# Kernel optimization log

Hardware: AMD Instinct MI355X
Metric: run time of the kernel (lower is better)

## Reference

```python
import jax, jax.numpy as jnp
import numpy as np

B, T, D, H, E, S, K = 2, 2048, 768, 1536, 8, 1, 2
STD = 0.02


def setup_inputs() -> dict:
    key = jax.random.key(0)
    ks = jax.random.split(key, 8)
    x = jax.random.normal(ks[0], (B, T, D), jnp.float32)
    router_w = jax.random.normal(ks[1], (E, D), jnp.float32) * STD
    sw1 = jax.random.normal(ks[2], (S, D, H), jnp.float32) * STD
    sw2 = jax.random.normal(ks[3], (S, D, H), jnp.float32) * STD
    sproj = jax.random.normal(ks[4], (S, H, D), jnp.float32) * STD
    ew1 = jax.random.normal(ks[5], (E, D, H), jnp.float32) * STD
    ew2 = jax.random.normal(ks[6], (E, D, H), jnp.float32) * STD
    eproj = jax.random.normal(ks[7], (E, H, D), jnp.float32) * STD
    return {"x": x, "router_w": router_w, "sw1": sw1, "sw2": sw2,
            "sproj": sproj, "ew1": ew1, "ew2": ew2, "eproj": eproj,
            "top_k": K}


def reference(x, router_w, sw1, sw2, sproj, ew1, ew2, eproj, top_k):
    n_experts = router_w.shape[0]
    # Shared experts (SwiGLU), summed over the shared-expert axis s.
    a = jnp.einsum('btd,sdh->bsth', x, sw1)
    b = jnp.einsum('btd,sdh->bsth', x, sw2)
    shared_out = jnp.einsum('bsth,shd->btd', jax.nn.silu(a) * b, sproj)  # [B,T,D]

    # Router: note the original applies softmax and calls the result `logits`,
    # returning it as the second output.
    probs = jax.nn.softmax(jnp.einsum('btd,ed->bte', x, router_w), axis=-1)  # [B,T,E]
    top_vals, top_idx = jax.lax.top_k(probs, top_k)
    weights = top_vals / jnp.sum(top_vals, axis=-1, keepdims=True)  # renormalized [B,T,K]

    # Dense combine weights: combine[b,t,e] = sum_k weights[b,t,k] * 1[top_idx[b,t,k]==e]
    combine = jnp.sum(jax.nn.one_hot(top_idx, n_experts, dtype=x.dtype)
                      * weights[..., None], axis=-2)  # [B,T,E]

    # Routed experts: compute every expert densely, then mask/weight by combine.
    ea = jnp.einsum('btd,edh->bteh', x, ew1)
    eb = jnp.einsum('btd,edh->bteh', x, ew2)
    routed = jnp.einsum('bteh,ehd,bte->btd', jax.nn.silu(ea) * eb, eproj, combine)

    return shared_out + routed, probs
```

## Files before the change

kernel.cpp:

```cpp
#include <hip/hip_runtime.h>

typedef unsigned short u16;
typedef __bf16 bf16x8 __attribute__((ext_vector_type(8)));
typedef float f32x4 __attribute__((ext_vector_type(4)));

__device__ __forceinline__ u16 f2bf(float f) {
  union { float f; unsigned u; } v; v.f = f;
  return (u16)((v.u + 0x7fffu + ((v.u >> 16) & 1u)) >> 16);
}

#define GLDS16(g, l)                                                          \
  __builtin_amdgcn_global_load_lds(                                           \
      (const __attribute__((address_space(1))) void*)(g),                     \
      (__attribute__((address_space(3))) void*)(l), 16, 0, 0)

#define SBAR()  __builtin_amdgcn_s_barrier()
#define SCHED() __builtin_amdgcn_sched_barrier(0)
#define VMCNT(n) asm volatile("s_waitcnt vmcnt(" #n ")" ::: "memory")

#define NTOK 4096
#define DIM  768
#define HID  1536
#define NEXP 8
#define CAPR 10240
#define SHB  10240
#define NSLOT 14336
#define MAXT1 56
#define MAXT2 112

__global__ __launch_bounds__(256) void k_tr_all(const float* __restrict__ ew1,
                                                const float* __restrict__ sw1,
                                                const float* __restrict__ ew2,
                                                const float* __restrict__ sw2,
                                                const float* __restrict__ eproj,
                                                const float* __restrict__ sproj,
                                                u16* __restrict__ dstBase) {
  __shared__ u16 tile[64][65];
  constexpr size_t SL = (size_t)HID * DIM;
  const int z = blockIdx.z;
  const float* src;
  int R, C, bxx = blockIdx.x, byy = blockIdx.y;
  if (z < 9)       { src = (z < 8) ? ew1 + (size_t)z * SL : sw1; R = DIM; C = HID; }
  else if (z < 18) { const int q = z - 9;  src = (q < 8) ? ew2 + (size_t)q * SL : sw2; R = DIM; C = HID; }
  else             { const int q = z - 18; src = (q < 8) ? eproj + (size_t)q * SL : sproj;
                     R = HID; C = DIM; const int t = bxx; bxx = byy; byy = t; }
  u16* dst = dstBase + (size_t)z * SL;
  const int c0 = bxx * 64, r0 = byy * 64;
  const int tx = threadIdx.x, ty = threadIdx.y;
  #pragma unroll
  for (int i = 0; i < 16; i++)
    tile[ty + 4 * i][tx] = f2bf(src[(size_t)(r0 + ty + 4 * i) * C + c0 + tx]);
  __syncthreads();
  #pragma unroll
  for (int i = 0; i < 16; i++)
    dst[(size_t)(c0 + ty + 4 * i) * R + r0 + tx] = tile[tx][ty + 4 * i];
}

__global__ __launch_bounds__(64) void k_router(const float* __restrict__ x,
                                               const float* __restrict__ rw,
                                               float* __restrict__ probs,
                                               int* __restrict__ topIdx,
                                               float* __restrict__ topW,
                                               u16* __restrict__ xb) {
  const int t = blockIdx.x;
  const int lane = threadIdx.x;
  const float* xr = x + (size_t)t * DIM;
  u16* xbr = xb + (size_t)t * DIM;
  float acc[NEXP] = {0, 0, 0, 0, 0, 0, 0, 0};
  #pragma unroll
  for (int i = 0; i < DIM / 64; i++) {
    const int d = lane + 64 * i;
    const float xv = xr[d];
    xbr[d] = f2bf(xv);
    #pragma unroll
    for (int e = 0; e < NEXP; e++) acc[e] += xv * rw[e * DIM + d];
  }
  #pragma unroll
  for (int e = 0; e < NEXP; e++)
    #pragma unroll
    for (int s = 32; s > 0; s >>= 1) acc[e] += __shfl_xor(acc[e], s, 64);
  if (lane == 0) {
    float mx = acc[0];
    #pragma unroll
    for (int e = 1; e < NEXP; e++) mx = fmaxf(mx, acc[e]);
    float p[NEXP], sum = 0.f;
    #pragma unroll
    for (int e = 0; e < NEXP; e++) { p[e] = expf(acc[e] - mx); sum += p[e]; }
    const float inv = 1.f / sum;
    #pragma unroll
    for (int e = 0; e < NEXP; e++) p[e] *= inv;
    #pragma unroll
    for (int e = 0; e < NEXP; e++) probs[(size_t)t * NEXP + e] = p[e];
    int i1 = 0;
    #pragma unroll
    for (int e = 1; e < NEXP; e++) if (p[e] > p[i1]) i1 = e;
    int i2 = (i1 == 0) ? 1 : 0;
    #pragma unroll
    for (int e = 0; e < NEXP; e++) if (e != i1 && p[e] > p[i2]) i2 = e;
    const float s2 = 1.f / (p[i1] + p[i2]);
    topIdx[2 * t] = i1; topIdx[2 * t + 1] = i2;
    topW[2 * t] = p[i1] * s2; topW[2 * t + 1] = p[i2] * s2;
  }
}

__global__ __launch_bounds__(256) void k_build(const int* __restrict__ topIdx,
                                               const float* __restrict__ topW,
                                               int* __restrict__ listT,
                                               float* __restrict__ listW,
                                               int* __restrict__ listP,
                                               int* __restrict__ cnt) {
  const int e = blockIdx.x;
  const int tid = threadIdx.x, w = tid >> 6, lane = tid & 63;
  __shared__ int wt[4];
  int base = 0;
  for (int c = 0; c < NTOK / 256; ++c) {
    const int t = c * 256 + tid;
    const int i0 = topIdx[2 * t], i1 = topIdx[2 * t + 1];
    const int pr = (i0 == e) ? 1 : ((i1 == e) ? 2 : 0);
    const unsigned long long m = __ballot(pr != 0);
    const int wl = __popcll(m & ((1ull << lane) - 1ull));
    if (lane == 0) wt[w] = __popcll(m);
    __syncthreads();
    int wbase = 0;
    #pragma unroll
    for (int j = 0; j < 4; j++) if (j < w) wbase += wt[j];
    if (pr) {
      const int pos = base + wbase + wl;
      listT[e * NTOK + pos] = t;
      listW[e * NTOK + pos] = (pr == 1) ? topW[2 * t] : topW[2 * t + 1];
      listP[e * NTOK + pos] = pr;
    }
    base += wt[0] + wt[1] + wt[2] + wt[3];
    __syncthreads();
  }
  if (tid == 0) cnt[e] = base;
}

__global__ __launch_bounds__(256) void k_tilemap(const int* __restrict__ cnt,
                                                 const int* __restrict__ listT,
                                                 const float* __restrict__ listW,
                                                 const int* __restrict__ listP,
                                                 int* __restrict__ tE1, int* __restrict__ tM1,
                                                 int* __restrict__ tE2, int* __restrict__ tM2,
                                                 int* __restrict__ slotTok,
                                                 float* __restrict__ slotW,
                                                 int* __restrict__ tokSlot) {
  __shared__ int offPad[NEXP + 1];
  __shared__ int cs[NEXP];
  const int tid = threadIdx.x;
  if (tid == 0) {
    int tt = 0, acc = 0;
    for (int e = 0; e < NEXP; e++) {
      cs[e] = cnt[e];
      offPad[e] = acc;
      const int tiles = (cs[e] + 255) >> 8;
      for (int i = 0; i < tiles; i++) { tE1[tt] = e; tM1[tt] = acc + i * 256; tt++; }
      acc += tiles * 256;
    }
    offPad[NEXP] = acc;
    for (int i = 0; i < NTOK / 256; i++) { tE1[tt] = NEXP; tM1[tt] = SHB + i * 256; tt++; }
    for (; tt < MAXT1; tt++) { tE1[tt] = -1; tM1[tt] = 0; }
    for (int j = 0; j < MAXT1; j++) {
      tE2[2 * j] = tE1[j];     tM2[2 * j] = tM1[j];
      tE2[2 * j + 1] = tE1[j]; tM2[2 * j + 1] = tM1[j] + 128;
    }
  }
  __syncthreads();
  for (int s = tid; s < CAPR; s += 256) {
    int tok = 0; float wv = 0.f; int pp = 0;
    #pragma unroll
    for (int e = 0; e < NEXP; e++)
      if (s >= offPad[e] && s < offPad[e + 1]) {
        const int i = s - offPad[e];
        if (i < cs[e]) {
          tok = listT[e * NTOK + i];
          wv = listW[e * NTOK + i];
          pp = listP[e * NTOK + i];
        }
      }
    slotTok[s] = tok; slotW[s] = wv;
    if (pp) tokSlot[2 * tok + (pp - 1)] = s;
  }
  for (int s = tid; s < NTOK; s += 256) { slotTok[SHB + s] = s; slotW[SHB + s] = 1.f; }
}

__global__ __launch_bounds__(512, 2) void k_gemm1(const u16* __restrict__ xb,
                                                  const u16* __restrict__ w1t,
                                                  const u16* __restrict__ w2t,
                                                  const int* __restrict__ tE1,
                                                  const int* __restrict__ tM1,
                                                  const int* __restrict__ slotTok,
                                                  const float* __restrict__ slotW,
                                                  u16* __restrict__ hidden) {
  __shared__ alignas(16) u16 L[2][32768];
  const int bid = blockIdx.x;
  const int wgid = (bid & 7) * 84 + (bid >> 3);
  const int bx = wgid % MAXT1, by = wgid / MAXT1;
  const int e = tE1[bx];
  if (e < 0) return;
  const int m0 = tM1[bx];
  const int nBase = by * 128;
  constexpr size_t SL = (size_t)HID * DIM;
  const u16* w1 = w1t + (size_t)e * SL;
  const u16* w2 = w2t + (size_t)e * SL;
  const int tid = threadIdx.x, w = tid >> 6, lane = tid & 63;
  const int wr = w >> 1, wc = w & 1;

  const int srow = tid >> 2;
  const int kcol = ((tid & 3) ^ ((tid >> 3) & 3)) * 8;
  const int tokA0 = slotTok[m0 + srow];
  const int tokA1 = slotTok[m0 + 128 + srow];
  const u16* gA0 = xb + (size_t)tokA0 * DIM + kcol;
  const u16* gA1 = xb + (size_t)tokA1 * DIM + kcol;
  const u16* gB1 = w1 + (size_t)(nBase + srow) * DIM + kcol;
  const u16* gB2 = w2 + (size_t)(nBase + srow) * DIM + kcol;
  const int dA0 = tid * 8, dA1 = 4096 + tid * 8, dB = tid * 8;

  const int rl = lane & 15;
  const int kq = lane >> 4;
  const int aBase = (wr * 64 + rl) * 32 + (kq ^ ((rl >> 1) & 3)) * 8;
  const int bBase = (wc * 64 + rl) * 32 + (kq ^ ((rl >> 1) & 3)) * 8;

  f32x4 acc1[4][4], acc2[4][4];
  const f32x4 vz = {0.f, 0.f, 0.f, 0.f};
  #pragma unroll
  for (int m = 0; m < 4; m++)
    #pragma unroll
    for (int n = 0; n < 4; n++) { acc1[m][n] = vz; acc2[m][n] = vz; }

#define G1_STA(d, koff, kh) do {                                              \
    GLDS16(gA0 + (koff), &L[d][(kh) * 8192 + dA0]);                           \
    GLDS16(gA1 + (koff), &L[d][(kh) * 8192 + dA1]); } while (0)
#define G1_STB(d, koff, kh) do {                                              \
    GLDS16(gB1 + (koff), &L[d][16384 + (kh) * 4096 + dB]);                    \
    GLDS16(gB2 + (koff), &L[d][24576 + (kh) * 4096 + dB]); } while (0)
#define G1_RDB(d, kh) do { _Pragma("unroll")                                  \
    for (int n = 0; n < 4; n++) {                                             \
      b1v[n] = *(const bf16x8*)&L[d][16384 + (kh) * 4096 + bBase + n * 512];  \
      b2v[n] = *(const bf16x8*)&L[d][24576 + (kh) * 4096 + bBase + n * 512]; } } while (0)
#define G1_RDA(d, kh, mp) do { _Pragma("unroll")                              \
    for (int j = 0; j < 2; j++)                                               \
      av[j] = *(const bf16x8*)&L[d][(kh) * 8192 + aBase + ((mp) * 2 + j) * 512]; } while (0)
#define G1_MM(mp) do { __builtin_amdgcn_s_setprio(1);                         \
    _Pragma("unroll") for (int j = 0; j < 2; j++)                             \
      _Pragma("unroll") for (int n = 0; n < 4; n++) {                         \
        acc1[(mp) * 2 + j][n] = __builtin_amdgcn_mfma_f32_16x16x32_bf16(av[j], b1v[n], acc1[(mp) * 2 + j][n], 0, 0, 0); \
        acc2[(mp) * 2 + j][n] = __builtin_amdgcn_mfma_f32_16x16x32_bf16(av[j], b2v[n], acc2[(mp) * 2 + j][n], 0, 0, 0); } \
    __builtin_amdgcn_s_setprio(0); } while (0)

  G1_STA(0, 0, 0);  G1_STB(0, 0, 0);
  G1_STA(0, 32, 1); G1_STB(0, 32, 1);
  G1_STA(1, 64, 0); G1_STB(1, 64, 0);
  SCHED(); VMCNT(8); SBAR(); SCHED();

  bf16x8 av[2], b1v[4], b2v[4];
  for (int i = 0; i < 5; i++) {
    const int kOff = i * 128;
    G1_RDB(0, 0); G1_RDA(0, 0, 0); SCHED(); G1_STA(1, kOff + 96, 1); SCHED();
    G1_MM(0); SCHED(); SBAR(); SCHED();
    G1_RDA(0, 0, 1); SCHED(); G1_STB(1, kOff + 96, 1); SCHED();
    G1_MM(1); SCHED(); VMCNT(8); SBAR(); SCHED();
    G1_RDB(0, 1); G1_RDA(0, 1, 0); SCHED(); G1_STA(0, kOff + 128, 0); SCHED();
    G1_MM(0); SCHED(); SBAR(); SCHED();
    G1_RDA(0, 1, 1); SCHED(); G1_STB(0, kOff + 128, 0); SCHED();
    G1_MM(1); SCHED(); VMCNT(8); SBAR(); SCHED();
    G1_RDB(1, 0); G1_RDA(1, 0, 0); SCHED(); G1_STA(0, kOff + 160, 1); SCHED();
    G1_MM(0); SCHED(); SBAR(); SCHED();
    G1_RDA(1, 0, 1); SCHED(); G1_STB(0, kOff + 160, 1); SCHED();
    G1_MM(1); SCHED(); VMCNT(8); SBAR(); SCHED();
    G1_RDB(1, 1); G1_RDA(1, 1, 0); SCHED(); G1_STA(1, kOff + 192, 0); SCHED();
    G1_MM(0); SCHED(); SBAR(); SCHED();
    G1_RDA(1, 1, 1); SCHED(); G1_STB(1, kOff + 192, 0); SCHED();
    G1_MM(1); SCHED(); VMCNT(8); SBAR(); SCHED();
  }
  G1_RDB(0, 0); G1_RDA(0, 0, 0); SCHED(); G1_STA(1, 736, 1); SCHED();
  G1_MM(0); SCHED(); SBAR(); SCHED();
  G1_RDA(0, 0, 1); SCHED(); G1_STB(1, 736, 1); SCHED();
  G1_MM(1); SCHED(); VMCNT(8); SBAR(); SCHED();
  G1_RDB(0, 1); G1_RDA(0, 1, 0); SCHED(); G1_MM(0); SCHED(); SBAR(); SCHED();
  G1_RDA(0, 1, 1); SCHED(); G1_MM(1); SCHED(); VMCNT(4); SBAR(); SCHED();
  G1_RDB(1, 0); G1_RDA(1, 0, 0); SCHED(); G1_MM(0); SCHED(); SBAR(); SCHED();
  G1_RDA(1, 0, 1); SCHED(); G1_MM(1); SCHED(); VMCNT(0); SBAR(); SCHED();
  G1_RDB(1, 1); G1_RDA(1, 1, 0); SCHED(); G1_MM(0); SCHED(); SBAR(); SCHED();
  G1_RDA(1, 1, 1); SCHED(); G1_MM(1);
#undef G1_STA
#undef G1_STB
#undef G1_RDB
#undef G1_RDA
#undef G1_MM

  #pragma unroll
  for (int m = 0; m < 4; m++)
    #pragma unroll
    for (int r = 0; r < 4; r++) {
      const int slot = m0 + wr * 64 + m * 16 + (lane >> 4) * 4 + r;
      const float cwv = slotW[slot];
      #pragma unroll
      for (int n = 0; n < 4; n++) {
        const int hcol = nBase + wc * 64 + n * 16 + (lane & 15);
        const float v1 = acc1[m][n][r], v2 = acc2[m][n][r];
        hidden[(size_t)slot * HID + hcol] = f2bf((v1 / (1.f + __expf(-v1))) * v2 * cwv);
      }
    }
}

__global__ __launch_bounds__(256, 3) void k_gemm2(const u16* __restrict__ hid,
                                                  const u16* __restrict__ pjt,
                                                  const int* __restrict__ tE2,
                                                  const int* __restrict__ tM2,
                                                  float* __restrict__ g2) {
  __shared__ alignas(16) u16 As[3][4096];
  __shared__ alignas(16) u16 Bs[3][4096];
  const int bid = blockIdx.x;
  const int wgid = (bid & 7) * 84 + (bid >> 3);
  const int bx = wgid % MAXT2;
  const int by = wgid / MAXT2;
  const int e = tE2[bx];
  if (e < 0) return;
  const int m0 = tM2[bx];
  const int nBase = by * 128;
  constexpr size_t SL = (size_t)HID * DIM;
  const u16* pj = pjt + (size_t)e * SL;
  const int tid = threadIdx.x, w = tid >> 6, lane = tid & 63;
  const int wr = w >> 1, wc = w & 1;

  const int qrow = lane >> 2;
  const int col0 = ((lane & 3) ^ ((lane >> 3) & 3)) * 8;
  const u16* gA0 = hid + (size_t)(m0 + w * 32 + qrow) * HID + col0;
  const u16* gA1 = hid + (size_t)(m0 + w * 32 + 16 + qrow) * HID + col0;
  const u16* gBa = pj + (size_t)(nBase + w * 32 + qrow) * HID + col0;
  const u16* gBb = pj + (size_t)(nBase + w * 32 + 16 + qrow) * HID + col0;
  const int l0 = (w * 128 + lane) * 8, l1 = (w * 128 + lane + 64) * 8;

  f32x4 acc[4][4];
  const f32x4 vz = {0.f, 0.f, 0.f, 0.f};
  #pragma unroll
  for (int m = 0; m < 4; m++)
    #pragma unroll
    for (int n = 0; n < 4; n++) acc[m][n] = vz;

  const int rbase = lane & 15;
  const int swz = (lane >> 4) ^ ((rbase >> 1) & 3);
  const int aoffB = (wr * 64 + rbase) * 32 + swz * 8;
  const int boffB = (wc * 64 + rbase) * 32 + swz * 8;

#define G2_STAGE(buf, kk) do {                                                \
    GLDS16(gA0 + (kk), &As[buf][l0]); GLDS16(gA1 + (kk), &As[buf][l1]);       \
    GLDS16(gBa + (kk), &Bs[buf][l0]); GLDS16(gBb + (kk), &Bs[buf][l1]);       \
  } while (0)

#define G2_BODY(buf, vm, dostage, kk) do {                                    \
    SCHED(); VMCNT(vm); SBAR(); SCHED();                                      \
    if (dostage) { G2_STAGE((buf + 2) % 3, kk); SCHED(); }                    \
    bf16x8 av[4], bv[4];                                                      \
    _Pragma("unroll")                                                         \
    for (int m = 0; m < 4; m++) av[m] = *(const bf16x8*)&As[buf][aoffB + m * 512]; \
    _Pragma("unroll")                                                         \
    for (int n = 0; n < 4; n++) bv[n] = *(const bf16x8*)&Bs[buf][boffB + n * 512]; \
    __builtin_amdgcn_s_setprio(1);                                            \
    _Pragma("unroll")                                                         \
    for (int m = 0; m < 4; m++)                                               \
      _Pragma("unroll")                                                       \
      for (int n = 0; n < 4; n++)                                             \
        acc[m][n] = __builtin_amdgcn_mfma_f32_16x16x32_bf16(av[m], bv[n], acc[m][n], 0, 0, 0); \
    __builtin_amdgcn_s_setprio(0);                                            \
  } while (0)

  G2_STAGE(0, 0);  SCHED();
  G2_STAGE(1, 32); SCHED();
  for (int t = 0; t < 45; t += 3) {
    G2_BODY(0, 4, true, (t + 2) * 32);
    G2_BODY(1, 4, true, (t + 3) * 32);
    G2_BODY(2, 4, true, (t + 4) * 32);
  }
  G2_BODY(0, 4, true, 47 * 32);
  G2_BODY(1, 4, false, 0);
  G2_BODY(2, 0, false, 0);
#undef G2_BODY
#undef G2_STAGE

  #pragma unroll
  for (int m = 0; m < 4; m++)
    #pragma unroll
    for (int r = 0; r < 4; r++) {
      const int slot = m0 + wr * 64 + m * 16 + (lane >> 4) * 4 + r;
      #pragma unroll
      for (int n = 0; n < 4; n++) {
        const int dcol = nBase + wc * 64 + n * 16 + (lane & 15);
        g2[(size_t)slot * DIM + dcol] = acc[m][n][r];
      }
    }
}

__global__ __launch_bounds__(192) void k_combine(const float* __restrict__ g2,
                                                 const int* __restrict__ tokSlot,
                                                 float* __restrict__ out) {
  const int t = blockIdx.x, d4 = threadIdx.x;
  const int sA = tokSlot[2 * t], sB = tokSlot[2 * t + 1];
  const int lo = sA < sB ? sA : sB;
  const int hi = sA < sB ? sB : sA;
  const float4 a = ((const float4*)(g2 + (size_t)lo * DIM))[d4];
  const float4 b = ((const float4*)(g2 + (size_t)hi * DIM))[d4];
  const float4 c = ((const float4*)(g2 + (size_t)(SHB + t) * DIM))[d4];
  float4 o;
  o.x = a.x + b.x + c.x; o.y = a.y + b.y + c.y;
  o.z = a.z + b.z + c.z; o.w = a.w + b.w + c.w;
  ((float4*)(out + (size_t)t * DIM))[d4] = o;
}

extern "C" void kernel_launch(void* const* d_in, const int* in_sizes, int n_in,
                              void* d_out, int out_size, void* d_ws, size_t ws_size,
                              hipStream_t stream) {
  const float* x     = (const float*)d_in[0];
  const float* rw    = (const float*)d_in[1];
  const float* sw1   = (const float*)d_in[2];
  const float* sw2   = (const float*)d_in[3];
  const float* sproj = (const float*)d_in[4];
  const float* ew1   = (const float*)d_in[5];
  const float* ew2   = (const float*)d_in[6];
  const float* eproj = (const float*)d_in[7];
  float* out   = (float*)d_out;
  float* probs = out + (size_t)NTOK * DIM;

  constexpr size_t SL = (size_t)HID * DIM;
  constexpr size_t off_xb   = 0;
  constexpr size_t off_w1t  = 6291456;
  constexpr size_t off_w2t  = off_w1t + 2 * 9 * SL;
  constexpr size_t off_pjt  = off_w2t + 2 * 9 * SL;
  constexpr size_t off_hid  = off_pjt + 2 * 9 * SL;
  constexpr size_t off_g2   = off_hid + (size_t)NSLOT * HID * 2;
  constexpr size_t off_meta = off_g2 + (size_t)NSLOT * DIM * 4;

  char* ws = (char*)d_ws;
  u16*   xb   = (u16*)(ws + off_xb);
  u16*   w1t  = (u16*)(ws + off_w1t);
  u16*   w2t  = (u16*)(ws + off_w2t);
  u16*   pjt  = (u16*)(ws + off_pjt);
  u16*   hid  = (u16*)(ws + off_hid);
  float* g2   = (float*)(ws + off_g2);
  char*  meta = ws + off_meta;
  int*   topIdx  = (int*)meta;
  float* topW    = (float*)(meta + 32768);
  int*   listT   = (int*)(meta + 65536);
  float* listW   = (float*)(meta + 196608);
  int*   listP   = (int*)(meta + 327680);
  int*   cnt     = (int*)(meta + 458752);
  int*   tE1     = (int*)(meta + 459264);
  int*   tM1     = (int*)(meta + 459776);
  int*   tE2     = (int*)(meta + 460288);
  int*   tM2     = (int*)(meta + 460800);
  int*   slotTok = (int*)(meta + 461312);
  float* slotW   = (float*)(meta + 518656);
  int*   tokSlot = (int*)(meta + 576000);

  k_router<<<NTOK, 64, 0, stream>>>(x, rw, probs, topIdx, topW, xb);
  k_tr_all<<<dim3(HID / 64, DIM / 64, 27), dim3(64, 4), 0, stream>>>(
      ew1, sw1, ew2, sw2, eproj, sproj, w1t);

  k_build<<<NEXP, 256, 0, stream>>>(topIdx, topW, listT, listW, listP, cnt);
  k_tilemap<<<1, 256, 0, stream>>>(cnt, listT, listW, listP, tE1, tM1, tE2, tM2,
                                   slotTok, slotW, tokSlot);

  k_gemm1<<<MAXT1 * (HID / 128), 512, 0, stream>>>(xb, w1t, w2t, tE1, tM1,
                                                   slotTok, slotW, hid);
  k_gemm2<<<MAXT2 * (DIM / 128), 256, 0, stream>>>(hid, pjt, tE2, tM2, g2);
  k_combine<<<NTOK, 192, 0, stream>>>(g2, tokSlot, out);
}
```

Baseline: 215.3 us.

## Repipeline gemm2 with split-K double buffering, parallelize slot map, pack router

The gemm2 kernel drops the 3-stage 32-wide K pipeline and uses two 64-wide K buffers, each split into two halves. Loads for later halves are interleaved with MFMA work at a finer grain, and occupancy drops from 3 to 2 blocks per CU. The single-block tilemap kernel is split into a tiny map kernel plus a multi-block slot-fill kernel, so slot filling no longer runs on one workgroup. The router now packs four tokens per 256-thread block, which cuts the block count.

```diff
diff --git a/kernel.cpp b/kernel.cpp
--- a/kernel.cpp
+++ b/kernel.cpp
@@ -56,14 +56,14 @@
     dst[(size_t)(c0 + ty + 4 * i) * R + r0 + tx] = tile[tx][ty + 4 * i];
 }
 
-__global__ __launch_bounds__(64) void k_router(const float* __restrict__ x,
-                                               const float* __restrict__ rw,
-                                               float* __restrict__ probs,
-                                               int* __restrict__ topIdx,
-                                               float* __restrict__ topW,
-                                               u16* __restrict__ xb) {
-  const int t = blockIdx.x;
-  const int lane = threadIdx.x;
+__global__ __launch_bounds__(256) void k_router(const float* __restrict__ x,
+                                                const float* __restrict__ rw,
+                                                float* __restrict__ probs,
+                                                int* __restrict__ topIdx,
+                                                float* __restrict__ topW,
+                                                u16* __restrict__ xb) {
+  const int wv = threadIdx.x >> 6, lane = threadIdx.x & 63;
+  const int t = blockIdx.x * 4 + wv;
   const float* xr = x + (size_t)t * DIM;
   u16* xbr = xb + (size_t)t * DIM;
   float acc[NEXP] = {0, 0, 0, 0, 0, 0, 0, 0};
@@ -136,24 +136,15 @@
   if (tid == 0) cnt[e] = base;
 }
 
-__global__ __launch_bounds__(256) void k_tilemap(const int* __restrict__ cnt,
-                                                 const int* __restrict__ listT,
-                                                 const float* __restrict__ listW,
-                                                 const int* __restrict__ listP,
-                                                 int* __restrict__ tE1, int* __restrict__ tM1,
-                                                 int* __restrict__ tE2, int* __restrict__ tM2,
-                                                 int* __restrict__ slotTok,
-                                                 float* __restrict__ slotW,
-                                                 int* __restrict__ tokSlot) {
-  __shared__ int offPad[NEXP + 1];
-  __shared__ int cs[NEXP];
-  const int tid = threadIdx.x;
-  if (tid == 0) {
+__global__ __launch_bounds__(64) void k_maps(const int* __restrict__ cnt,
+                                             int* __restrict__ tE1, int* __restrict__ tM1,
+                                             int* __restrict__ tE2, int* __restrict__ tM2,
+                                             int* __restrict__ offPad) {
+  if (threadIdx.x == 0) {
     int tt = 0, acc = 0;
     for (int e = 0; e < NEXP; e++) {
-      cs[e] = cnt[e];
       offPad[e] = acc;
-      const int tiles = (cs[e] + 255) >> 8;
+      const int tiles = (cnt[e] + 255) >> 8;
       for (int i = 0; i < tiles; i++) { tE1[tt] = e; tM1[tt] = acc + i * 256; tt++; }
       acc += tiles * 256;
     }
@@ -165,13 +156,28 @@
       tE2[2 * j + 1] = tE1[j]; tM2[2 * j + 1] = tM1[j] + 128;
     }
   }
+}
+
+__global__ __launch_bounds__(256) void k_slots(const int* __restrict__ offPad,
+                                               const int* __restrict__ cnt,
+                                               const int* __restrict__ listT,
+                                               const float* __restrict__ listW,
+                                               const int* __restrict__ listP,
+                                               int* __restrict__ slotTok,
+                                               float* __restrict__ slotW,
+                                               int* __restrict__ tokSlot) {
+  __shared__ int op[NEXP + 1];
+  __shared__ int cs[NEXP];
+  if (threadIdx.x < NEXP + 1) op[threadIdx.x] = offPad[threadIdx.x];
+  if (threadIdx.x < NEXP) cs[threadIdx.x] = cnt[threadIdx.x];
   __syncthreads();
-  for (int s = tid; s < CAPR; s += 256) {
+  const int s = blockIdx.x * 256 + threadIdx.x;
+  if (s < CAPR) {
     int tok = 0; float wv = 0.f; int pp = 0;
     #pragma unroll
     for (int e = 0; e < NEXP; e++)
-      if (s >= offPad[e] && s < offPad[e + 1]) {
-        const int i = s - offPad[e];
+      if (s >= op[e] && s < op[e + 1]) {
+        const int i = s - op[e];
         if (i < cs[e]) {
           tok = listT[e * NTOK + i];
           wv = listW[e * NTOK + i];
@@ -180,8 +186,10 @@
       }
     slotTok[s] = tok; slotW[s] = wv;
     if (pp) tokSlot[2 * tok + (pp - 1)] = s;
-  }
-  for (int s = tid; s < NTOK; s += 256) { slotTok[SHB + s] = s; slotW[SHB + s] = 1.f; }
+  } else {
+    const int t = s - CAPR;
+    slotTok[SHB + t] = t; slotW[SHB + t] = 1.f;
+  }
 }
 
 __global__ __launch_bounds__(512, 2) void k_gemm1(const u16* __restrict__ xb,
@@ -304,17 +312,15 @@
     }
 }
 
-__global__ __launch_bounds__(256, 3) void k_gemm2(const u16* __restrict__ hid,
+__global__ __launch_bounds__(256, 2) void k_gemm2(const u16* __restrict__ hid,
                                                   const u16* __restrict__ pjt,
                                                   const int* __restrict__ tE2,
                                                   const int* __restrict__ tM2,
                                                   float* __restrict__ g2) {
-  __shared__ alignas(16) u16 As[3][4096];
-  __shared__ alignas(16) u16 Bs[3][4096];
+  __shared__ alignas(16) u16 L[2][16384];
   const int bid = blockIdx.x;
   const int wgid = (bid & 7) * 84 + (bid >> 3);
-  const int bx = wgid % MAXT2;
-  const int by = wgid / MAXT2;
+  const int bx = wgid % MAXT2, by = wgid / MAXT2;
   const int e = tE2[bx];
   if (e < 0) return;
   const int m0 = tM2[bx];
@@ -324,13 +330,18 @@
   const int tid = threadIdx.x, w = tid >> 6, lane = tid & 63;
   const int wr = w >> 1, wc = w & 1;
 
-  const int qrow = lane >> 2;
-  const int col0 = ((lane & 3) ^ ((lane >> 3) & 3)) * 8;
-  const u16* gA0 = hid + (size_t)(m0 + w * 32 + qrow) * HID + col0;
-  const u16* gA1 = hid + (size_t)(m0 + w * 32 + 16 + qrow) * HID + col0;
-  const u16* gBa = pj + (size_t)(nBase + w * 32 + qrow) * HID + col0;
-  const u16* gBb = pj + (size_t)(nBase + w * 32 + 16 + qrow) * HID + col0;
-  const int l0 = (w * 128 + lane) * 8, l1 = (w * 128 + lane + 64) * 8;
+  const int r0 = tid >> 2;
+  const int kcol = ((tid & 3) ^ ((tid >> 3) & 3)) * 8;
+  const u16* gA0 = hid + (size_t)(m0 + r0) * HID + kcol;
+  const u16* gA1 = hid + (size_t)(m0 + 64 + r0) * HID + kcol;
+  const u16* gB0 = pj + (size_t)(nBase + r0) * HID + kcol;
+  const u16* gB1p = pj + (size_t)(nBase + 64 + r0) * HID + kcol;
+  const int d0 = tid * 8, d1 = 2048 + tid * 8;
+
+  const int rl = lane & 15;
+  const int kq = lane >> 4;
+  const int aBase = (wr * 64 + rl) * 32 + (kq ^ ((rl >> 1) & 3)) * 8;
+  const int bBase = (wc * 64 + rl) * 32 + (kq ^ ((rl >> 1) & 3)) * 8;
 
   f32x4 acc[4][4];
   const f32x4 vz = {0.f, 0.f, 0.f, 0.f};
@@ -339,45 +350,64 @@
     #pragma unroll
     for (int n = 0; n < 4; n++) acc[m][n] = vz;
 
-  const int rbase = lane & 15;
-  const int swz = (lane >> 4) ^ ((rbase >> 1) & 3);
-  const int aoffB = (wr * 64 + rbase) * 32 + swz * 8;
-  const int boffB = (wc * 64 + rbase) * 32 + swz * 8;
-
-#define G2_STAGE(buf, kk) do {                                                \
-    GLDS16(gA0 + (kk), &As[buf][l0]); GLDS16(gA1 + (kk), &As[buf][l1]);       \
-    GLDS16(gBa + (kk), &Bs[buf][l0]); GLDS16(gBb + (kk), &Bs[buf][l1]);       \
-  } while (0)
-
-#define G2_BODY(buf, vm, dostage, kk) do {                                    \
-    SCHED(); VMCNT(vm); SBAR(); SCHED();                                      \
-    if (dostage) { G2_STAGE((buf + 2) % 3, kk); SCHED(); }                    \
-    bf16x8 av[4], bv[4];                                                      \
-    _Pragma("unroll")                                                         \
-    for (int m = 0; m < 4; m++) av[m] = *(const bf16x8*)&As[buf][aoffB + m * 512]; \
-    _Pragma("unroll")                                                         \
-    for (int n = 0; n < 4; n++) bv[n] = *(const bf16x8*)&Bs[buf][boffB + n * 512]; \
-    __builtin_amdgcn_s_setprio(1);                                            \
-    _Pragma("unroll")                                                         \
-    for (int m = 0; m < 4; m++)                                               \
-      _Pragma("unroll")                                                       \
-      for (int n = 0; n < 4; n++)                                             \
-        acc[m][n] = __builtin_amdgcn_mfma_f32_16x16x32_bf16(av[m], bv[n], acc[m][n], 0, 0, 0); \
-    __builtin_amdgcn_s_setprio(0);                                            \
-  } while (0)
-
-  G2_STAGE(0, 0);  SCHED();
-  G2_STAGE(1, 32); SCHED();
-  for (int t = 0; t < 45; t += 3) {
-    G2_BODY(0, 4, true, (t + 2) * 32);
-    G2_BODY(1, 4, true, (t + 3) * 32);
-    G2_BODY(2, 4, true, (t + 4) * 32);
-  }
-  G2_BODY(0, 4, true, 47 * 32);
-  G2_BODY(1, 4, false, 0);
-  G2_BODY(2, 0, false, 0);
-#undef G2_BODY
-#undef G2_STAGE
+#define G2_STA(d, koff, kh) do {                                              \
+    GLDS16(gA0 + (koff), &L[d][(kh) * 4096 + d0]);                            \
+    GLDS16(gA1 + (koff), &L[d][(kh) * 4096 + d1]); } while (0)
+#define G2_STB(d, koff, kh) do {                                              \
+    GLDS16(gB0 + (koff), &L[d][8192 + (kh) * 4096 + d0]);                     \
+    GLDS16(gB1p + (koff), &L[d][8192 + (kh) * 4096 + d1]); } while (0)
+#define G2_RDB(d, kh) do { _Pragma("unroll")                                  \
+    for (int n = 0; n < 4; n++)                                               \
+      bv[n] = *(const bf16x8*)&L[d][8192 + (kh) * 4096 + bBase + n * 512]; } while (0)
+#define G2_RDA(d, kh, mp) do { _Pragma("unroll")                              \
+    for (int j = 0; j < 2; j++)                                               \
+      av[j] = *(const bf16x8*)&L[d][(kh) * 4096 + aBase + ((mp) * 2 + j) * 512]; } while (0)
+#define G2_MM(mp) do { __builtin_amdgcn_s_setprio(1);                         \
+    _Pragma("unroll") for (int j = 0; j < 2; j++)                             \
+      _Pragma("unroll") for (int n = 0; n < 4; n++)                           \
+        acc[(mp) * 2 + j][n] = __builtin_amdgcn_mfma_f32_16x16x32_bf16(av[j], bv[n], acc[(mp) * 2 + j][n], 0, 0, 0); \
+    __builtin_amdgcn_s_setprio(0); } while (0)
+
+  G2_STA(0, 0, 0);  G2_STB(0, 0, 0);
+  G2_STA(0, 32, 1); G2_STB(0, 32, 1);
+  G2_STA(1, 64, 0); G2_STB(1, 64, 0);
+  SCHED(); VMCNT(8); SBAR(); SCHED();
+
+  bf16x8 av[2], bv[4];
+  for (int i = 0; i < 11; i++) {
+    const int kOff = i * 128;
+    G2_RDB(0, 0); G2_RDA(0, 0, 0); SCHED(); G2_STA(1, kOff + 96, 1); SCHED();
+    G2_MM(0); SCHED(); SBAR(); SCHED();
+    G2_RDA(0, 0, 1); SCHED(); G2_STB(1, kOff + 96, 1); SCHED();
+    G2_MM(1); SCHED(); VMCNT(8); SBAR(); SCHED();
+    G2_RDB(0, 1); G2_RDA(0, 1, 0); SCHED(); G2_STA(0, kOff + 128, 0); SCHED();
+    G2_MM(0); SCHED(); SBAR(); SCHED();
+    G2_RDA(0, 1, 1); SCHED(); G2_STB(0, kOff + 128, 0); SCHED();
+    G2_MM(1); SCHED(); VMCNT(8); SBAR(); SCHED();
+    G2_RDB(1, 0); G2_RDA(1, 0, 0); SCHED(); G2_STA(0, kOff + 160, 1); SCHED();
+    G2_MM(0); SCHED(); SBAR(); SCHED();
+    G2_RDA(1, 0, 1); SCHED(); G2_STB(0, kOff + 160, 1); SCHED();
+    G2_MM(1); SCHED(); VMCNT(8); SBAR(); SCHED();
+    G2_RDB(1, 1); G2_RDA(1, 1, 0); SCHED(); G2_STA(1, kOff + 192, 0); SCHED();
+    G2_MM(0); SCHED(); SBAR(); SCHED();
+    G2_RDA(1, 1, 1); SCHED(); G2_STB(1, kOff + 192, 0); SCHED();
+    G2_MM(1); SCHED(); VMCNT(8); SBAR(); SCHED();
+  }
+  G2_RDB(0, 0); G2_RDA(0, 0, 0); SCHED(); G2_STA(1, 1504, 1); SCHED();
+  G2_MM(0); SCHED(); SBAR(); SCHED();
+  G2_RDA(0, 0, 1); SCHED(); G2_STB(1, 1504, 1); SCHED();
+  G2_MM(1); SCHED(); VMCNT(8); SBAR(); SCHED();
+  G2_RDB(0, 1); G2_RDA(0, 1, 0); SCHED(); G2_MM(0); SCHED(); SBAR(); SCHED();
+  G2_RDA(0, 1, 1); SCHED(); G2_MM(1); SCHED(); VMCNT(4); SBAR(); SCHED();
+  G2_RDB(1, 0); G2_RDA(1, 0, 0); SCHED(); G2_MM(0); SCHED(); SBAR(); SCHED();
+  G2_RDA(1, 0, 1); SCHED(); G2_MM(1); SCHED(); VMCNT(0); SBAR(); SCHED();
+  G2_RDB(1, 1); G2_RDA(1, 1, 0); SCHED(); G2_MM(0); SCHED(); SBAR(); SCHED();
+  G2_RDA(1, 1, 1); SCHED(); G2_MM(1);
+#undef G2_STA
+#undef G2_STB
+#undef G2_RDB
+#undef G2_RDA
+#undef G2_MM
 
   #pragma unroll
   for (int m = 0; m < 4; m++)
@@ -452,14 +482,16 @@
   int*   slotTok = (int*)(meta + 461312);
   float* slotW   = (float*)(meta + 518656);
   int*   tokSlot = (int*)(meta + 576000);
-
-  k_router<<<NTOK, 64, 0, stream>>>(x, rw, probs, topIdx, topW, xb);
+  int*   offPad  = (int*)(meta + 608768);
+
+  k_router<<<NTOK / 4, 256, 0, stream>>>(x, rw, probs, topIdx, topW, xb);
   k_tr_all<<<dim3(HID / 64, DIM / 64, 27), dim3(64, 4), 0, stream>>>(
       ew1, sw1, ew2, sw2, eproj, sproj, w1t);
 
   k_build<<<NEXP, 256, 0, stream>>>(topIdx, topW, listT, listW, listP, cnt);
-  k_tilemap<<<1, 256, 0, stream>>>(cnt, listT, listW, listP, tE1, tM1, tE2, tM2,
-                                   slotTok, slotW, tokSlot);
+  k_maps<<<1, 64, 0, stream>>>(cnt, tE1, tM1, tE2, tM2, offPad);
+  k_slots<<<NSLOT / 256, 256, 0, stream>>>(offPad, cnt, listT, listW, listP,
+                                           slotTok, slotW, tokSlot);
 
   k_gemm1<<<MAXT1 * (HID / 128), 512, 0, stream>>>(xb, w1t, w2t, tE1, tM1,
                                                    slotTok, slotW, hid);
```

Measured after the change: 198.3 us. 1.09x faster.
